# Kernel tuning notes

Measured on AMD Instinct MI355X. Metric: run time of the kernel, lower is better.

## Reference

```python
import jax, jax.numpy as jnp
import numpy as np

EPS = 1e-5  # torch LayerNorm default


def _ln(x, w, b):
    m = jnp.mean(x, axis=-1, keepdims=True)
    v = jnp.mean((x - m) ** 2, axis=-1, keepdims=True)
    return (x - m) / jnp.sqrt(v + EPS) * w + b


def _conv1x1(x, w, b):
    # x: [B,C,H,W], w: [O,C], b: [O]
    return jnp.einsum('bchw,oc->bohw', x, w) + b[None, :, None, None]


def setup_inputs() -> dict:
    key = jax.random.key(0)
    ks = jax.random.split(key, 5)
    B, Cin, H, W = 8, 384, 64, 64
    D, N = 128, 512
    s = lambda k, shape, scale=0.02: jax.random.normal(k, shape, jnp.float32) * scale
    return {
        'x': jax.random.normal(ks[0], (B, Cin, H, W), jnp.float32),
        'DR': jax.random.normal(ks[1], (N, D), jnp.float32),
        'conv_in_w': s(ks[2], (D, Cin)),
        'conv_in_b': jnp.zeros((D,), jnp.float32),
        'sem_w': s(ks[3], (D, D)),
        'sem_b': jnp.zeros((D,), jnp.float32),
        'norm1_w': jnp.ones((D,), jnp.float32),
        'norm1_b': jnp.zeros((D,), jnp.float32),
        'norm2_w': jnp.ones((D,), jnp.float32),
        'norm2_b': jnp.zeros((D,), jnp.float32),
        'conv_out_w': s(ks[4], (Cin, D)),
        'conv_out_b': jnp.zeros((Cin,), jnp.float32),
    }


def reference(x, DR, conv_in_w, conv_in_b, sem_w, sem_b, norm1_w, norm1_b,
              norm2_w, norm2_b, conv_out_w, conv_out_b):
    B, _, H, W = x.shape
    N = DR.shape[0]
    x_align = _conv1x1(x, conv_in_w, conv_in_b)                      # [B,D,H,W]
    x_sem = _conv1x1(x_align, sem_w, sem_b)                          # semantic_extra (1x1 conv)
    x_sem = x_sem.transpose(0, 2, 3, 1).reshape(B, H * W, -1)        # [B,HW,D]
    x_sem = _ln(x_sem, norm1_w, norm1_b)
    dr = _ln(DR, norm2_w, norm2_b).T                                 # [D,N] (same for all batches)
    # NOTE: original applies norm_1 TWICE for the numerator (faithful quirk)
    c_u = jnp.einsum('bld,dn->bln', _ln(x_sem, norm1_w, norm1_b), dr)  # [B,HW,N]
    c_d_l = jnp.sqrt(jnp.sum(x_sem ** 2, axis=-1, keepdims=True))      # [B,HW,1]
    c_d_r = jnp.sqrt(jnp.sum(dr ** 2, axis=0, keepdims=True))[None]    # [1,1,N]
    sim = c_u / (c_d_l * c_d_r)
    sim_soft = jax.nn.softmax(sim, axis=-1)                          # [B,HW,N]
    sim2d = sim_soft.transpose(0, 2, 1).reshape(B, N, H, W)
    degrad = jnp.einsum('bln,dn->bdl', sim_soft, dr).reshape(B, -1, H, W)  # [B,D,H,W]
    # pow-mask with per-batch min-max normalization
    mask_v = jnp.max(sim2d ** 3, axis=1, keepdims=True)              # [B,1,H,W]
    mn = jnp.min(mask_v.reshape(B, -1), axis=1).reshape(B, 1, 1, 1)
    mx = jnp.max(mask_v.reshape(B, -1), axis=1).reshape(B, 1, 1, 1)
    mask_v = 1.0 - (mask_v - mn) / (mx - mn)
    # topk row selection (torch fancy indexing gives [B,B,K,N]; squeeze(1) is a no-op for B>1)
    max_values = jnp.max(sim_soft, axis=2)                           # [B,HW]
    K = (H * W) // 50
    _, top_idx = jax.lax.top_k(max_values, K)                        # [B,K]
    results = jnp.take(sim_soft, top_idx, axis=1)                    # [B,B,K,N]
    out_img = _conv1x1(degrad, conv_out_w, conv_out_b)               # [B,Cin,H,W]
    return (mask_v, out_img, results)
```

## Files before the change

### kernel.cpp

```cpp
#include <hip/hip_runtime.h>
#include <cstdint>

#define EPS 1e-5f
#define BB   8
#define CIN  384
#define HWs  4096
#define LT   32768
#define DD   128
#define NN   512
#define TOPK 81

typedef short short8 __attribute__((ext_vector_type(8)));
typedef float f32x4  __attribute__((ext_vector_type(4)));

__device__ __forceinline__ unsigned short f2bf(float x) {
  unsigned u = __float_as_uint(x);
  u += 0x7fffu + ((u >> 16) & 1u);
  return (unsigned short)(u >> 16);
}
__device__ __forceinline__ float bf2f(unsigned u16) {
  return __uint_as_float(u16 << 16);
}
__device__ __forceinline__ void put_frag(unsigned short* buf, int tile, int rc, int k, float v) {
  int ks = k >> 5, g = (k >> 3) & 3, j = k & 7;
  int basehw = ((tile * 4 + ks) * 2) * 512 + (g * 16 + rc) * 8 + j;
  unsigned short hi = f2bf(v);
  buf[basehw] = hi;
  buf[basehw + 512] = f2bf(v - bf2f(hi));
}

__global__ __launch_bounds__(64) void k_dr(const float* __restrict__ DR,
    const float* __restrict__ w2, const float* __restrict__ b2,
    const float* __restrict__ w1, const float* __restrict__ b1,
    unsigned short* __restrict__ drwF, unsigned short* __restrict__ drlnF,
    float* __restrict__ t2, float* __restrict__ rcr) {
  int n = blockIdx.x;
  int lane = threadIdx.x;
  const float* row = DR + n * DD;
  float x0 = row[lane], x1 = row[lane + 64];
  float s = x0 + x1, sq = x0 * x0 + x1 * x1;
  #pragma unroll
  for (int o = 32; o; o >>= 1) { s += __shfl_xor(s, o); sq += __shfl_xor(sq, o); }
  float m = s * (1.f / 128.f);
  float v = sq * (1.f / 128.f) - m * m;
  float inv = rsqrtf(v + EPS);
  float y0 = (x0 - m) * inv * w2[lane] + b2[lane];
  float y1 = (x1 - m) * inv * w2[lane + 64] + b2[lane + 64];
  int nt = n >> 4, cc = n & 15;
  put_frag(drwF, nt, cc, lane, y0 * w1[lane]);
  put_frag(drwF, nt, cc, lane + 64, y1 * w1[lane + 64]);
  int ks = n >> 5, gB = (n >> 3) & 3, j = n & 7;
  {
    int d = lane;
    unsigned short hi = f2bf(y0);
    int base = (((d >> 4) * 16 + ks) * 2) * 512 + (gB * 16 + (d & 15)) * 8 + j;
    drlnF[base] = hi;
    drlnF[base + 512] = f2bf(y0 - bf2f(hi));
  }
  {
    int d = lane + 64;
    unsigned short hi = f2bf(y1);
    int base = (((d >> 4) * 16 + ks) * 2) * 512 + (gB * 16 + (d & 15)) * 8 + j;
    drlnF[base] = hi;
    drlnF[base + 512] = f2bf(y1 - bf2f(hi));
  }
  float pt2 = y0 * b1[lane] + y1 * b1[lane + 64];
  float pss = y0 * y0 + y1 * y1;
  #pragma unroll
  for (int o = 32; o; o >>= 1) { pt2 += __shfl_xor(pt2, o); pss += __shfl_xor(pss, o); }
  if (lane == 0) { t2[n] = pt2; rcr[n] = rsqrtf(pss); }
}

__global__ __launch_bounds__(256) void k_bprep(const float* __restrict__ src,
                                               unsigned short* __restrict__ dst,
                                               int K) {
  int rt = blockIdx.x, kb = blockIdx.y;
  int t = threadIdx.x, m = t >> 4, kg = t & 15;
  int k0 = kb * 128 + kg * 8;
  const float* s = src + (size_t)(rt * 16 + m) * K + k0;
  float4 f0 = *(const float4*)s;
  float4 f1 = *(const float4*)(s + 4);
  float vs[8] = {f0.x, f0.y, f0.z, f0.w, f1.x, f1.y, f1.z, f1.w};
  short8 hi, lo;
  #pragma unroll
  for (int j = 0; j < 8; ++j) {
    unsigned short h = f2bf(vs[j]);
    hi[j] = (short)h;
    lo[j] = (short)f2bf(vs[j] - bf2f(h));
  }
  int nkt = K >> 5;
  int ks = k0 >> 5, g = (k0 >> 3) & 3;
  short8* D8 = (short8*)dst;
  int base = ((rt * nkt + ks) * 2) * 64 + g * 16 + m;
  D8[base] = hi;
  D8[base + 64] = lo;
}

__global__ __launch_bounds__(256) void k_convin(const float* __restrict__ x,
    const unsigned short* __restrict__ WinF, const float* __restrict__ bias,
    unsigned short* __restrict__ xaF) {
  __shared__ float smem[64 * 132];
  int t = threadIdx.x;
  int w = t >> 6, lane = t & 63, m = lane & 15, g = lane >> 4;
  int l0 = blockIdx.x * 64;
  int b = l0 >> 12, hw0 = l0 & 4095;
  const float* xb = x + (size_t)b * CIN * HWs + hw0;
  const short8* B8 = (const short8*)WinF;
  f32x4 acc[4][2];
  #pragma unroll
  for (int lt = 0; lt < 4; ++lt)
    #pragma unroll
    for (int j2 = 0; j2 < 2; ++j2) acc[lt][j2] = (f32x4){0.f, 0.f, 0.f, 0.f};
  for (int ks = 0; ks < 12; ++ks) {
    short8 ah[4], al[4];
    const float* xc = xb + (size_t)(ks * 32 + g * 8) * HWs;
    #pragma unroll
    for (int lt = 0; lt < 4; ++lt) {
      const float* xcl = xc + lt * 16 + m;
      float v[8];
      #pragma unroll
      for (int j = 0; j < 8; ++j) v[j] = xcl[(size_t)j * HWs];
      #pragma unroll
      for (int j = 0; j < 8; ++j) {
        unsigned short h = f2bf(v[j]);
        ah[lt][j] = (short)h;
        al[lt][j] = (short)f2bf(v[j] - bf2f(h));
      }
    }
    #pragma unroll
    for (int j2 = 0; j2 < 2; ++j2) {
      int dt = w * 2 + j2;
      short8 bh = B8[((dt * 12 + ks) * 2 + 0) * 64 + lane];
      short8 bl = B8[((dt * 12 + ks) * 2 + 1) * 64 + lane];
      #pragma unroll
      for (int lt = 0; lt < 4; ++lt) {
        acc[lt][j2] = __builtin_amdgcn_mfma_f32_16x16x32_bf16(ah[lt], bh, acc[lt][j2], 0, 0, 0);
        acc[lt][j2] = __builtin_amdgcn_mfma_f32_16x16x32_bf16(ah[lt], bl, acc[lt][j2], 0, 0, 0);
        acc[lt][j2] = __builtin_amdgcn_mfma_f32_16x16x32_bf16(al[lt], bh, acc[lt][j2], 0, 0, 0);
      }
    }
  }
  float bia[2] = {bias[w * 32 + m], bias[w * 32 + 16 + m]};
  #pragma unroll
  for (int lt = 0; lt < 4; ++lt)
    #pragma unroll
    for (int j2 = 0; j2 < 2; ++j2)
      #pragma unroll
      for (int r = 0; r < 4; ++r)
        smem[(lt * 16 + g * 4 + r) * 132 + (w * 2 + j2) * 16 + m] = acc[lt][j2][r] + bia[j2];
  __syncthreads();
  short8* X8 = (short8*)xaF;
  #pragma unroll
  for (int it = 0; it < 4; ++it) {
    int idx = it * 256 + t;
    int l = idx & 63, dq = idx >> 6;
    const float* src = &smem[l * 132 + dq * 8];
    float4 f0 = *(const float4*)src;
    float4 f1 = *(const float4*)(src + 4);
    float vs[8] = {f0.x, f0.y, f0.z, f0.w, f1.x, f1.y, f1.z, f1.w};
    short8 hi, lo;
    #pragma unroll
    for (int j = 0; j < 8; ++j) {
      unsigned short h = f2bf(vs[j]);
      hi[j] = (short)h;
      lo[j] = (short)f2bf(vs[j] - bf2f(h));
    }
    int ltg = (l0 + l) >> 4;
    int idx8 = ((ltg * 4 + (dq >> 2)) * 2) * 64 + (dq & 3) * 16 + (l & 15);
    X8[idx8] = hi;
    X8[idx8 + 64] = lo;
  }
}

__global__ __launch_bounds__(256) void k_sem(const unsigned short* __restrict__ xaF,
    const unsigned short* __restrict__ semWF, const float* __restrict__ bias,
    const float* __restrict__ w1, const float* __restrict__ b1,
    unsigned short* __restrict__ ApF, float* __restrict__ rclv) {
  __shared__ float smem[64 * 132];
  __shared__ float sredS[64][4], sredQ[64][4];
  __shared__ float rowM[64], rowI[64];
  int t = threadIdx.x;
  int w = t >> 6, lane = t & 63, m = lane & 15, g = lane >> 4;
  int l0 = blockIdx.x * 64;
  int lt0 = l0 >> 4;
  const short8* A8 = (const short8*)xaF;
  const short8* B8 = (const short8*)semWF;
  f32x4 acc[4][2];
  #pragma unroll
  for (int lt = 0; lt < 4; ++lt)
    #pragma unroll
    for (int j2 = 0; j2 < 2; ++j2) acc[lt][j2] = (f32x4){0.f, 0.f, 0.f, 0.f};
  #pragma unroll
  for (int ks = 0; ks < 4; ++ks) {
    short8 ah[4], al[4];
    #pragma unroll
    for (int lt = 0; lt < 4; ++lt) {
      ah[lt] = A8[(((lt0 + lt) * 4 + ks) * 2 + 0) * 64 + lane];
      al[lt] = A8[(((lt0 + lt) * 4 + ks) * 2 + 1) * 64 + lane];
    }
    #pragma unroll
    for (int j2 = 0; j2 < 2; ++j2) {
      int dt = w * 2 + j2;
      short8 bh = B8[((dt * 4 + ks) * 2 + 0) * 64 + lane];
      short8 bl = B8[((dt * 4 + ks) * 2 + 1) * 64 + lane];
      #pragma unroll
      for (int lt = 0; lt < 4; ++lt) {
        acc[lt][j2] = __builtin_amdgcn_mfma_f32_16x16x32_bf16(ah[lt], bh, acc[lt][j2], 0, 0, 0);
        acc[lt][j2] = __builtin_amdgcn_mfma_f32_16x16x32_bf16(ah[lt], bl, acc[lt][j2], 0, 0, 0);
        acc[lt][j2] = __builtin_amdgcn_mfma_f32_16x16x32_bf16(al[lt], bh, acc[lt][j2], 0, 0, 0);
      }
    }
  }
  float bia[2] = {bias[w * 32 + m], bias[w * 32 + 16 + m]};
  #pragma unroll
  for (int lt = 0; lt < 4; ++lt)
    #pragma unroll
    for (int j2 = 0; j2 < 2; ++j2)
      #pragma unroll
      for (int r = 0; r < 4; ++r) acc[lt][j2][r] += bia[j2];
  float s1[4][4], q1[4][4];
  #pragma unroll
  for (int lt = 0; lt < 4; ++lt)
    #pragma unroll
    for (int r = 0; r < 4; ++r) {
      float a = acc[lt][0][r], b2v = acc[lt][1][r];
      s1[lt][r] = a + b2v;
      q1[lt][r] = a * a + b2v * b2v;
    }
  #pragma unroll
  for (int o = 1; o < 16; o <<= 1)
    #pragma unroll
    for (int lt = 0; lt < 4; ++lt)
      #pragma unroll
      for (int r = 0; r < 4; ++r) {
        s1[lt][r] += __shfl_xor(s1[lt][r], o);
        q1[lt][r] += __shfl_xor(q1[lt][r], o);
      }
  if (m == 0) {
    #pragma unroll
    for (int lt = 0; lt < 4; ++lt)
      #pragma unroll
      for (int r = 0; r < 4; ++r) {
        sredS[lt * 16 + g * 4 + r][w] = s1[lt][r];
        sredQ[lt * 16 + g * 4 + r][w] = q1[lt][r];
      }
  }
  __syncthreads();
  if (t < 64) {
    float S = sredS[t][0] + sredS[t][1] + sredS[t][2] + sredS[t][3];
    float Q = sredQ[t][0] + sredQ[t][1] + sredQ[t][2] + sredQ[t][3];
    float mu = S * (1.f / 128.f);
    float var = Q * (1.f / 128.f) - mu * mu;
    rowM[t] = mu;
    rowI[t] = rsqrtf(var + EPS);
  }
  __syncthreads();
  float w1v[2] = {w1[w * 32 + m], w1[w * 32 + 16 + m]};
  float b1v[2] = {b1[w * 32 + m], b1[w * 32 + 16 + m]};
  #pragma unroll
  for (int lt = 0; lt < 4; ++lt)
    #pragma unroll
    for (int r = 0; r < 4; ++r) {
      float mu = rowM[lt * 16 + g * 4 + r];
      float iv = rowI[lt * 16 + g * 4 + r];
      float y0 = (acc[lt][0][r] - mu) * iv * w1v[0] + b1v[0];
      float y1 = (acc[lt][1][r] - mu) * iv * w1v[1] + b1v[1];
      acc[lt][0][r] = y0; acc[lt][1][r] = y1;
      s1[lt][r] = y0 + y1;
      q1[lt][r] = y0 * y0 + y1 * y1;
    }
  #pragma unroll
  for (int o = 1; o < 16; o <<= 1)
    #pragma unroll
    for (int lt = 0; lt < 4; ++lt)
      #pragma unroll
      for (int r = 0; r < 4; ++r) {
        s1[lt][r] += __shfl_xor(s1[lt][r], o);
        q1[lt][r] += __shfl_xor(q1[lt][r], o);
      }
  if (m == 0) {
    #pragma unroll
    for (int lt = 0; lt < 4; ++lt)
      #pragma unroll
      for (int r = 0; r < 4; ++r) {
        sredS[lt * 16 + g * 4 + r][w] = s1[lt][r];
        sredQ[lt * 16 + g * 4 + r][w] = q1[lt][r];
      }
  }
  __syncthreads();
  if (t < 64) {
    float S = sredS[t][0] + sredS[t][1] + sredS[t][2] + sredS[t][3];
    float Q = sredQ[t][0] + sredQ[t][1] + sredQ[t][2] + sredQ[t][3];
    float m2 = S * (1.f / 128.f);
    float v2 = Q * (1.f / 128.f) - m2 * m2;
    float inv2 = rsqrtf(v2 + EPS);
    float rcl = rsqrtf(Q);
    rowM[t] = m2;
    rowI[t] = inv2 * rcl;
    rclv[l0 + t] = rcl;
  }
  __syncthreads();
  #pragma unroll
  for (int lt = 0; lt < 4; ++lt)
    #pragma unroll
    for (int r = 0; r < 4; ++r) {
      float m2 = rowM[lt * 16 + g * 4 + r];
      float sc = rowI[lt * 16 + g * 4 + r];
      smem[(lt * 16 + g * 4 + r) * 132 + w * 32 + m] = (acc[lt][0][r] - m2) * sc;
      smem[(lt * 16 + g * 4 + r) * 132 + w * 32 + 16 + m] = (acc[lt][1][r] - m2) * sc;
    }
  __syncthreads();
  short8* O8 = (short8*)ApF;
  #pragma unroll
  for (int it = 0; it < 4; ++it) {
    int idx = it * 256 + t;
    int l = idx & 63, dq = idx >> 6;
    const float* src = &smem[l * 132 + dq * 8];
    float4 f0 = *(const float4*)src;
    float4 f1 = *(const float4*)(src + 4);
    float vs[8] = {f0.x, f0.y, f0.z, f0.w, f1.x, f1.y, f1.z, f1.w};
    short8 hi, lo;
    #pragma unroll
    for (int j = 0; j < 8; ++j) {
      unsigned short h = f2bf(vs[j]);
      hi[j] = (short)h;
      lo[j] = (short)f2bf(vs[j] - bf2f(h));
    }
    int ltg = (l0 + l) >> 4;
    int idx8 = ((ltg * 4 + (dq >> 2)) * 2) * 64 + (dq & 3) * 16 + (l & 15);
    O8[idx8] = hi;
    O8[idx8 + 64] = lo;
  }
}

__global__ __launch_bounds__(256) void k_scores(const unsigned short* __restrict__ ApF,
    const unsigned short* __restrict__ drwF, const float* __restrict__ t2g,
    const float* __restrict__ rcrg, const float* __restrict__ rclg,
    unsigned short* __restrict__ pF, float* __restrict__ maxv) {
  __shared__ float sred[32][5];
  int t = threadIdx.x;
  int w = t >> 6, lane = t & 63, c = lane & 15, g = lane >> 4;
  int l0 = blockIdx.x * 32;
  int lt0 = blockIdx.x * 2;
  const short8* A8 = (const short8*)ApF;
  const short8* B8 = (const short8*)drwF;
  f32x4 acc[2][8];
  #pragma unroll
  for (int il = 0; il < 2; ++il)
    #pragma unroll
    for (int jn = 0; jn < 8; ++jn) acc[il][jn] = (f32x4){0.f, 0.f, 0.f, 0.f};
  #pragma unroll
  for (int ks = 0; ks < 4; ++ks) {
    short8 ah0 = A8[((lt0 * 4 + ks) * 2 + 0) * 64 + lane];
    short8 al0 = A8[((lt0 * 4 + ks) * 2 + 1) * 64 + lane];
    short8 ah1 = A8[(((lt0 + 1) * 4 + ks) * 2 + 0) * 64 + lane];
    short8 al1 = A8[(((lt0 + 1) * 4 + ks) * 2 + 1) * 64 + lane];
    #pragma unroll
    for (int jn = 0; jn < 8; ++jn) {
      int nt = w * 8 + jn;
      short8 bh = B8[((nt * 4 + ks) * 2 + 0) * 64 + lane];
      short8 bl = B8[((nt * 4 + ks) * 2 + 1) * 64 + lane];
      acc[0][jn] = __builtin_amdgcn_mfma_f32_16x16x32_bf16(ah0, bh, acc[0][jn], 0, 0, 0);
      acc[0][jn] = __builtin_amdgcn_mfma_f32_16x16x32_bf16(ah0, bl, acc[0][jn], 0, 0, 0);
      acc[0][jn] = __builtin_amdgcn_mfma_f32_16x16x32_bf16(al0, bh, acc[0][jn], 0, 0, 0);
      acc[1][jn] = __builtin_amdgcn_mfma_f32_16x16x32_bf16(ah1, bh, acc[1][jn], 0, 0, 0);
      acc[1][jn] = __builtin_amdgcn_mfma_f32_16x16x32_bf16(ah1, bl, acc[1][jn], 0, 0, 0);
      acc[1][jn] = __builtin_amdgcn_mfma_f32_16x16x32_bf16(al1, bh, acc[1][jn], 0, 0, 0);
    }
  }
  float rcrv[8], t2v[8];
  #pragma unroll
  for (int jn = 0; jn < 8; ++jn) {
    int n = w * 128 + jn * 16 + c;
    rcrv[jn] = rcrg[n]; t2v[jn] = t2g[n];
  }
  float rclr[2][4];
  #pragma unroll
  for (int il = 0; il < 2; ++il)
    #pragma unroll
    for (int r = 0; r < 4; ++r)
      rclr[il][r] = rclg[l0 + il * 16 + g * 4 + r];
  float M[2][4];
  #pragma unroll
  for (int il = 0; il < 2; ++il)
    #pragma unroll
    for (int r = 0; r < 4; ++r) M[il][r] = -1e30f;
  #pragma unroll
  for (int il = 0; il < 2; ++il)
    #pragma unroll
    for (int jn = 0; jn < 8; ++jn) {
      f32x4 a = acc[il][jn];
      #pragma unroll
      for (int r = 0; r < 4; ++r) {
        float s = rcrv[jn] * (a[r] + rclr[il][r] * t2v[jn]);
        a[r] = s;
        M[il][r] = fmaxf(M[il][r], s);
      }
      acc[il][jn] = a;
    }
  #pragma unroll
  for (int o = 1; o < 16; o <<= 1)
    #pragma unroll
    for (int il = 0; il < 2; ++il)
      #pragma unroll
      for (int r = 0; r < 4; ++r)
        M[il][r] = fmaxf(M[il][r], __shfl_xor(M[il][r], o));
  if (c == 0) {
    #pragma unroll
    for (int il = 0; il < 2; ++il)
      #pragma unroll
      for (int r = 0; r < 4; ++r)
        sred[il * 16 + g * 4 + r][w] = M[il][r];
  }
  __syncthreads();
  if (t < 32) {
    float mm = fmaxf(fmaxf(sred[t][0], sred[t][1]), fmaxf(sred[t][2], sred[t][3]));
    sred[t][4] = mm;
  }
  __syncthreads();
  float Mf[2][4];
  #pragma unroll
  for (int il = 0; il < 2; ++il)
    #pragma unroll
    for (int r = 0; r < 4; ++r)
      Mf[il][r] = sred[il * 16 + g * 4 + r][4];
  float S[2][4];
  #pragma unroll
  for (int il = 0; il < 2; ++il)
    #pragma unroll
    for (int r = 0; r < 4; ++r) S[il][r] = 0.f;
  #pragma unroll
  for (int il = 0; il < 2; ++il)
    #pragma unroll
    for (int jn = 0; jn < 8; ++jn) {
      f32x4 a = acc[il][jn];
      #pragma unroll
      for (int r = 0; r < 4; ++r) {
        float e = expf(a[r] - Mf[il][r]);
        a[r] = e;
        S[il][r] += e;
      }
      acc[il][jn] = a;
    }
  #pragma unroll
  for (int o = 1; o < 16; o <<= 1)
    #pragma unroll
    for (int il = 0; il < 2; ++il)
      #pragma unroll
      for (int r = 0; r < 4; ++r)
        S[il][r] += __shfl_xor(S[il][r], o);
  __syncthreads();
  if (c == 0) {
    #pragma unroll
    for (int il = 0; il < 2; ++il)
      #pragma unroll
      for (int r = 0; r < 4; ++r)
        sred[il * 16 + g * 4 + r][w] = S[il][r];
  }
  __syncthreads();
  if (t < 32) {
    float tot = sred[t][0] + sred[t][1] + sred[t][2] + sred[t][3];
    float rs = 1.f / tot;
    sred[t][4] = rs;
    maxv[l0 + t] = rs;
  }
  __syncthreads();
  #pragma unroll
  for (int il = 0; il < 2; ++il) {
    int lt = lt0 + il;
    #pragma unroll
    for (int r = 0; r < 4; ++r) {
      int mrow = g * 4 + r;
      float rs = sred[il * 16 + mrow][4];
      #pragma unroll
      for (int jn = 0; jn < 8; ++jn) {
        int ks = w * 4 + (jn >> 1);
        int gB = (jn * 2 + (c >> 3)) & 3;
        pF[((lt * 16 + ks) * 64 + gB * 16 + mrow) * 8 + (c & 7)] =
            f2bf(acc[il][jn][r] * rs);
      }
    }
  }
}

__global__ __launch_bounds__(256) void k_deg(const unsigned short* __restrict__ pF,
    const unsigned short* __restrict__ drlnF, const unsigned short* __restrict__ WoF,
    const float* __restrict__ bo, float* __restrict__ out_img) {
  __shared__ float smem[64 * 132];
  int t = threadIdx.x;
  int w = t >> 6, lane = t & 63, c = lane & 15, g = lane >> 4;
  int l0 = blockIdx.x * 64;
  int lt0 = l0 >> 4;
  const short8* P8 = (const short8*)pF;
  const short8* D8 = (const short8*)drlnF;
  const short8* W8 = (const short8*)WoF;
  f32x4 acc[4][2];
  #pragma unroll
  for (int lt = 0; lt < 4; ++lt)
    #pragma unroll
    for (int j2 = 0; j2 < 2; ++j2) acc[lt][j2] = (f32x4){0.f, 0.f, 0.f, 0.f};
  for (int ks = 0; ks < 16; ++ks) {
    short8 a0 = P8[((lt0 + 0) * 16 + ks) * 64 + lane];
    short8 a1 = P8[((lt0 + 1) * 16 + ks) * 64 + lane];
    short8 a2 = P8[((lt0 + 2) * 16 + ks) * 64 + lane];
    short8 a3 = P8[((lt0 + 3) * 16 + ks) * 64 + lane];
    #pragma unroll
    for (int j2 = 0; j2 < 2; ++j2) {
      int dt = w * 2 + j2;
      short8 bh = D8[((dt * 16 + ks) * 2 + 0) * 64 + lane];
      short8 bl = D8[((dt * 16 + ks) * 2 + 1) * 64 + lane];
      acc[0][j2] = __builtin_amdgcn_mfma_f32_16x16x32_bf16(a0, bh, acc[0][j2], 0, 0, 0);
      acc[0][j2] = __builtin_amdgcn_mfma_f32_16x16x32_bf16(a0, bl, acc[0][j2], 0, 0, 0);
      acc[1][j2] = __builtin_amdgcn_mfma_f32_16x16x32_bf16(a1, bh, acc[1][j2], 0, 0, 0);
      acc[1][j2] = __builtin_amdgcn_mfma_f32_16x16x32_bf16(a1, bl, acc[1][j2], 0, 0, 0);
      acc[2][j2] = __builtin_amdgcn_mfma_f32_16x16x32_bf16(a2, bh, acc[2][j2], 0, 0, 0);
      acc[2][j2] = __builtin_amdgcn_mfma_f32_16x16x32_bf16(a2, bl, acc[2][j2], 0, 0, 0);
      acc[3][j2] = __builtin_amdgcn_mfma_f32_16x16x32_bf16(a3, bh, acc[3][j2], 0, 0, 0);
      acc[3][j2] = __builtin_amdgcn_mfma_f32_16x16x32_bf16(a3, bl, acc[3][j2], 0, 0, 0);
    }
  }
  #pragma unroll
  for (int lt = 0; lt < 4; ++lt)
    #pragma unroll
    for (int j2 = 0; j2 < 2; ++j2)
      #pragma unroll
      for (int r = 0; r < 4; ++r)
        smem[(lt * 16 + g * 4 + r) * 132 + w * 32 + j2 * 16 + c] = acc[lt][j2][r];
  __syncthreads();
  f32x4 acc2[4][6];
  #pragma unroll
  for (int lt = 0; lt < 4; ++lt)
    #pragma unroll
    for (int ot = 0; ot < 6; ++ot) acc2[lt][ot] = (f32x4){0.f, 0.f, 0.f, 0.f};
  #pragma unroll
  for (int ks2 = 0; ks2 < 4; ++ks2) {
    short8 dh[4];
    #pragma unroll
    for (int lt = 0; lt < 4; ++lt) {
      const float* src = &smem[(lt * 16 + c) * 132 + ks2 * 32 + g * 8];
      float4 f0 = *(const float4*)src;
      float4 f1 = *(const float4*)(src + 4);
      float vs[8] = {f0.x, f0.y, f0.z, f0.w, f1.x, f1.y, f1.z, f1.w};
      #pragma unroll
      for (int j = 0; j < 8; ++j) dh[lt][j] = (short)f2bf(vs[j]);
    }
    #pragma unroll
    for (int ot = 0; ot < 6; ++ot) {
      int otg = w * 6 + ot;
      short8 wh = W8[((otg * 4 + ks2) * 2 + 0) * 64 + lane];
      short8 wl = W8[((otg * 4 + ks2) * 2 + 1) * 64 + lane];
      #pragma unroll
      for (int lt = 0; lt < 4; ++lt) {
        acc2[lt][ot] = __builtin_amdgcn_mfma_f32_16x16x32_bf16(dh[lt], wh, acc2[lt][ot], 0, 0, 0);
        acc2[lt][ot] = __builtin_amdgcn_mfma_f32_16x16x32_bf16(dh[lt], wl, acc2[lt][ot], 0, 0, 0);
      }
    }
  }
  __syncthreads();
  int b = l0 >> 12, hw0 = l0 & 4095;
  float* ob = out_img + (size_t)b * CIN * HWs + hw0;
  float bov[6];
  #pragma unroll
  for (int ot = 0; ot < 6; ++ot) bov[ot] = bo[w * 96 + ot * 16 + c];
  for (int ot = 0; ot < 6; ++ot) {
    #pragma unroll
    for (int lt = 0; lt < 4; ++lt)
      #pragma unroll
      for (int r = 0; r < 4; ++r)
        smem[(lt * 16 + g * 4 + r) * 65 + w * 16 + c] = acc2[lt][ot][r] + bov[ot];
    __syncthreads();
    #pragma unroll
    for (int i = 0; i < 16; ++i) {
      int idx = t + i * 256;
      int o_l = idx >> 6, ll = idx & 63;
      int o = (o_l >> 4) * 96 + ot * 16 + (o_l & 15);
      ob[(size_t)o * HWs + ll] = smem[ll * 65 + o_l];
    }
    __syncthreads();
  }
}

__global__ __launch_bounds__(256) void k_mask(const float* __restrict__ maxv,
                                              float* __restrict__ outm) {
  int b = blockIdx.x, t = threadIdx.x;
  float c[16];
  float mn = 1e30f, mx = -1e30f;
  #pragma unroll
  for (int j = 0; j < 16; ++j) {
    float x = maxv[b * HWs + t + j * 256];
    float cc = x * x * x;
    c[j] = cc;
    mn = fminf(mn, cc); mx = fmaxf(mx, cc);
  }
  #pragma unroll
  for (int o = 32; o; o >>= 1) { mn = fminf(mn, __shfl_xor(mn, o)); mx = fmaxf(mx, __shfl_xor(mx, o)); }
  __shared__ float smn[4], smx[4];
  int w = t >> 6;
  if ((t & 63) == 0) { smn[w] = mn; smx[w] = mx; }
  __syncthreads();
  mn = fminf(fminf(smn[0], smn[1]), fminf(smn[2], smn[3]));
  mx = fmaxf(fmaxf(smx[0], smx[1]), fmaxf(smx[2], smx[3]));
  float sc = 1.f / (mx - mn);
  #pragma unroll
  for (int j = 0; j < 16; ++j)
    outm[b * HWs + t + j * 256] = 1.f - (c[j] - mn) * sc;
}

__global__ __launch_bounds__(256) void k_topk(const float* __restrict__ maxv,
                                              int* __restrict__ tix) {
  __shared__ unsigned int hist[4][256];
  __shared__ unsigned long long slist[TOPK];
  __shared__ unsigned long long bc_prefix;
  __shared__ int bc_need, scount;
  int b = blockIdx.x, t = threadIdx.x;
  int w = t >> 6;
  unsigned long long key[16];
  #pragma unroll
  for (int j = 0; j < 16; ++j) {
    int idx = t + j * 256;
    unsigned int bits = __float_as_uint(maxv[b * HWs + idx]);
    key[j] = ((unsigned long long)bits << 12) | (unsigned)(4095 - idx);
  }
  if (t == 0) { bc_prefix = 0ull; bc_need = TOPK; scount = 0; }
  for (int r = 0; r < 6; ++r) {
    int shift = 40 - 8 * r;
    unsigned int* hflat = (unsigned int*)hist;
    hflat[t] = 0; hflat[t + 256] = 0; hflat[t + 512] = 0; hflat[t + 768] = 0;
    __syncthreads();
    unsigned long long prefix = bc_prefix;
    int bins[16];
    #pragma unroll
    for (int j = 0; j < 16; ++j)
      bins[j] = ((key[j] >> (shift + 8)) == prefix) ? (int)((key[j] >> shift) & 255) : -1;
    #pragma unroll
    for (int j = 0; j < 16; ++j) {
      if (bins[j] >= 0) {
        int cnt = 1;
        #pragma unroll
        for (int j2 = j + 1; j2 < 16; ++j2)
          if (bins[j2] == bins[j]) { bins[j2] = -1; ++cnt; }
        atomicAdd(&hist[w][bins[j]], (unsigned)cnt);
      }
    }
    __syncthreads();
    if (t < 64) {
      int cb[4], s = 0;
      #pragma unroll
      for (int j = 0; j < 4; ++j) {
        int bin = 255 - (t * 4 + j);
        cb[j] = (int)(hist[0][bin] + hist[1][bin] + hist[2][bin] + hist[3][bin]);
        s += cb[j];
      }
      int P = s;
      #pragma unroll
      for (int o = 1; o < 64; o <<= 1) {
        int u = __shfl_up(P, o);
        if (t >= o) P += u;
      }
      int need = bc_need;
      unsigned long long mask = __ballot(P >= need);
      int first = __ffsll((long long)mask) - 1;
      if (t == first) {
        int acc = P - s;
        #pragma unroll
        for (int j = 0; j < 4; ++j) {
          if (acc + cb[j] >= need) {
            bc_prefix = (prefix << 8) | (unsigned)(255 - (t * 4 + j));
            bc_need = need - acc;
            break;
          }
          acc += cb[j];
        }
      }
    }
    __syncthreads();
  }
  unsigned long long K81 = bc_prefix;
  #pragma unroll
  for (int j = 0; j < 16; ++j)
    if (key[j] >= K81) {
      int pos = atomicAdd(&scount, 1);
      slist[pos] = key[j];
    }
  __syncthreads();
  if (t < TOPK) {
    unsigned long long mine = slist[t];
    int rank = 0;
    for (int i = 0; i < TOPK; ++i) rank += (slist[i] > mine) ? 1 : 0;
    tix[b * TOPK + rank] = 4095 - (int)(mine & 0xFFFull);
  }
}

__global__ __launch_bounds__(128) void k_gather(const unsigned short* __restrict__ pF,
    const int* __restrict__ tix, float* __restrict__ outr) {
  int gB_ = blockIdx.x;
  int k = gB_ % TOPK;
  int bb = gB_ / TOPK;
  int b2 = bb & 7, b = bb >> 3;
  int l = b * HWs + tix[b2 * TOPK + k];
  int lt = l >> 4, mrow = l & 15;
  int t = threadIdx.x;
  int ks = t >> 3, gq = (t >> 1) & 3, j0 = (t & 1) * 4;
  int base = ((lt * 16 + ks) * 64 + gq * 16 + mrow) * 8 + j0;
  const unsigned* src = (const unsigned*)(pF + base);
  unsigned u0 = src[0], u1 = src[1];
  float4 v = {bf2f(u0 & 0xffffu), bf2f(u0 >> 16), bf2f(u1 & 0xffffu), bf2f(u1 >> 16)};
  *(float4*)(outr + (size_t)gB_ * NN + t * 4) = v;
}

extern "C" void kernel_launch(void* const* d_in, const int* in_sizes, int n_in,
                              void* d_out, int out_size, void* d_ws, size_t ws_size,
                              hipStream_t stream) {
  const float* x    = (const float*)d_in[0];
  const float* DR   = (const float*)d_in[1];
  const float* win  = (const float*)d_in[2];
  const float* bin  = (const float*)d_in[3];
  const float* sw   = (const float*)d_in[4];
  const float* sb   = (const float*)d_in[5];
  const float* n1w  = (const float*)d_in[6];
  const float* n1b  = (const float*)d_in[7];
  const float* n2w  = (const float*)d_in[8];
  const float* n2b  = (const float*)d_in[9];
  const float* wout = (const float*)d_in[10];
  const float* bout = (const float*)d_in[11];
  float* out = (float*)d_out;
  float* W = (float*)d_ws;

  unsigned short* drwF  = (unsigned short*)(W);
  float* t2   = W + 65536;
  float* rcr  = W + 66048;
  float* rclv = W + 66560;
  float* maxv = W + 99328;
  unsigned short* drlnF = (unsigned short*)(W + 132096);
  unsigned short* WoF   = (unsigned short*)(W + 197632);
  unsigned short* WinF  = (unsigned short*)(W + 246784);
  unsigned short* semWF = (unsigned short*)(W + 295936);
  unsigned short* ApF   = (unsigned short*)(W + 312320);
  unsigned short* xaF   = (unsigned short*)(W + 4506624);
  unsigned short* pF    = (unsigned short*)(W + 4506624);
  int*   tix  = (int*)(W + 12895232);

  float* out_mask = out;
  float* out_img  = out + 32768;
  float* out_res  = out + 32768 + 12582912;

  k_dr    <<<NN, 64, 0, stream>>>(DR, n2w, n2b, n1w, n1b, drwF, drlnF, t2, rcr);
  k_bprep <<<dim3(8, 3),  256, 0, stream>>>(win,  WinF,  CIN);
  k_bprep <<<dim3(8, 1),  256, 0, stream>>>(sw,   semWF, DD);
  k_bprep <<<dim3(24, 1), 256, 0, stream>>>(wout, WoF,   DD);
  k_convin<<<512,  256, 0, stream>>>(x, WinF, bin, xaF);
  k_sem   <<<512,  256, 0, stream>>>(xaF, semWF, sb, n1w, n1b, ApF, rclv);
  k_scores<<<1024, 256, 0, stream>>>(ApF, drwF, t2, rcr, rclv, pF, maxv);
  k_deg   <<<512,  256, 0, stream>>>(pF, drlnF, WoF, bout, out_img);
  k_mask  <<<BB,   256, 0, stream>>>(maxv, out_mask);
  k_topk  <<<BB,   256, 0, stream>>>(maxv, tix);
  k_gather<<<BB * BB * TOPK, 128, 0, stream>>>(pF, tix, out_res);
}
```

Baseline: 250.1 us.

## Fuse prep and mask/topk kernels, enlarge score tiles with LDS-staged output

Merges the DR layernorm kernel and the three weight-prep launches into one 184-block kernel, and merges the mask and top-k kernels into one, cutting launch count. The score kernel now handles 64 rows per block instead of 32, doubling reuse of the B fragments. It uses a single-pass online-softmax merge across waves in place of two separate barrier-separated reductions. Probabilities are staged in LDS and written out as coalesced 16-byte stores. The costs are higher register pressure from 32 accumulators, about 66KB of shared memory per block, and fewer blocks in the score grid.

Result: no change. 251.9 us (+0.7%).

```diff
diff --git a/kernel.cpp b/kernel.cpp
--- a/kernel.cpp
+++ b/kernel.cpp
@@ -29,53 +29,67 @@
   buf[basehw + 512] = f2bf(v - bf2f(hi));
 }
 
-__global__ __launch_bounds__(64) void k_dr(const float* __restrict__ DR,
+__global__ __launch_bounds__(256) void k_prep(const float* __restrict__ DR,
     const float* __restrict__ w2, const float* __restrict__ b2,
     const float* __restrict__ w1, const float* __restrict__ b1,
+    const float* __restrict__ win, const float* __restrict__ sw,
+    const float* __restrict__ wout,
     unsigned short* __restrict__ drwF, unsigned short* __restrict__ drlnF,
-    float* __restrict__ t2, float* __restrict__ rcr) {
-  int n = blockIdx.x;
-  int lane = threadIdx.x;
-  const float* row = DR + n * DD;
-  float x0 = row[lane], x1 = row[lane + 64];
-  float s = x0 + x1, sq = x0 * x0 + x1 * x1;
-  #pragma unroll
-  for (int o = 32; o; o >>= 1) { s += __shfl_xor(s, o); sq += __shfl_xor(sq, o); }
-  float m = s * (1.f / 128.f);
-  float v = sq * (1.f / 128.f) - m * m;
-  float inv = rsqrtf(v + EPS);
-  float y0 = (x0 - m) * inv * w2[lane] + b2[lane];
-  float y1 = (x1 - m) * inv * w2[lane + 64] + b2[lane + 64];
-  int nt = n >> 4, cc = n & 15;
-  put_frag(drwF, nt, cc, lane, y0 * w1[lane]);
-  put_frag(drwF, nt, cc, lane + 64, y1 * w1[lane + 64]);
-  int ks = n >> 5, gB = (n >> 3) & 3, j = n & 7;
-  {
-    int d = lane;
-    unsigned short hi = f2bf(y0);
-    int base = (((d >> 4) * 16 + ks) * 2) * 512 + (gB * 16 + (d & 15)) * 8 + j;
-    drlnF[base] = hi;
-    drlnF[base + 512] = f2bf(y0 - bf2f(hi));
-  }
-  {
-    int d = lane + 64;
-    unsigned short hi = f2bf(y1);
-    int base = (((d >> 4) * 16 + ks) * 2) * 512 + (gB * 16 + (d & 15)) * 8 + j;
-    drlnF[base] = hi;
-    drlnF[base + 512] = f2bf(y1 - bf2f(hi));
-  }
-  float pt2 = y0 * b1[lane] + y1 * b1[lane + 64];
-  float pss = y0 * y0 + y1 * y1;
-  #pragma unroll
-  for (int o = 32; o; o >>= 1) { pt2 += __shfl_xor(pt2, o); pss += __shfl_xor(pss, o); }
-  if (lane == 0) { t2[n] = pt2; rcr[n] = rsqrtf(pss); }
-}
-
-__global__ __launch_bounds__(256) void k_bprep(const float* __restrict__ src,
-                                               unsigned short* __restrict__ dst,
-                                               int K) {
-  int rt = blockIdx.x, kb = blockIdx.y;
-  int t = threadIdx.x, m = t >> 4, kg = t & 15;
+    float* __restrict__ t2, float* __restrict__ rcr,
+    unsigned short* __restrict__ WinF, unsigned short* __restrict__ semWF,
+    unsigned short* __restrict__ WoF) {
+  int blk = blockIdx.x;
+  int t = threadIdx.x;
+  if (blk < 128) {
+    int w = t >> 6, lane = t & 63;
+    int n = blk * 4 + w;
+    const float* row = DR + n * DD;
+    float x0 = row[lane], x1 = row[lane + 64];
+    float s = x0 + x1, sq = x0 * x0 + x1 * x1;
+    #pragma unroll
+    for (int o = 32; o; o >>= 1) { s += __shfl_xor(s, o); sq += __shfl_xor(sq, o); }
+    float m = s * (1.f / 128.f);
+    float v = sq * (1.f / 128.f) - m * m;
+    float inv = rsqrtf(v + EPS);
+    float y0 = (x0 - m) * inv * w2[lane] + b2[lane];
+    float y1 = (x1 - m) * inv * w2[lane + 64] + b2[lane + 64];
+    int nt = n >> 4, cc = n & 15;
+    put_frag(drwF, nt, cc, lane, y0 * w1[lane]);
+    put_frag(drwF, nt, cc, lane + 64, y1 * w1[lane + 64]);
+    int ks = n >> 5, gB = (n >> 3) & 3, j = n & 7;
+    {
+      int d = lane;
+      unsigned short hi = f2bf(y0);
+      int base = (((d >> 4) * 16 + ks) * 2) * 512 + (gB * 16 + (d & 15)) * 8 + j;
+      drlnF[base] = hi;
+      drlnF[base + 512] = f2bf(y0 - bf2f(hi));
+    }
+    {
+      int d = lane + 64;
+      unsigned short hi = f2bf(y1);
+      int base = (((d >> 4) * 16 + ks) * 2) * 512 + (gB * 16 + (d & 15)) * 8 + j;
+      drlnF[base] = hi;
+      drlnF[base + 512] = f2bf(y1 - bf2f(hi));
+    }
+    float pt2 = y0 * b1[lane] + y1 * b1[lane + 64];
+    float pss = y0 * y0 + y1 * y1;
+    #pragma unroll
+    for (int o = 32; o; o >>= 1) { pt2 += __shfl_xor(pt2, o); pss += __shfl_xor(pss, o); }
+    if (lane == 0) { t2[n] = pt2; rcr[n] = rsqrtf(pss); }
+    return;
+  }
+  const float* src;
+  unsigned short* dst;
+  int K, rt, kb = 0;
+  if (blk < 152) {
+    int idx = blk - 128;
+    rt = idx & 7; kb = idx >> 3; src = win; dst = WinF; K = CIN;
+  } else if (blk < 160) {
+    rt = blk - 152; src = sw; dst = semWF; K = DD;
+  } else {
+    rt = blk - 160; src = wout; dst = WoF; K = DD;
+  }
+  int m = t >> 4, kg = t & 15;
   int k0 = kb * 128 + kg * 8;
   const float* s = src + (size_t)(rt * 16 + m) * K + k0;
   float4 f0 = *(const float4*)s;
@@ -337,35 +351,38 @@
     const unsigned short* __restrict__ drwF, const float* __restrict__ t2g,
     const float* __restrict__ rcrg, const float* __restrict__ rclg,
     unsigned short* __restrict__ pF, float* __restrict__ maxv) {
-  __shared__ float sred[32][5];
+  __shared__ unsigned short pS[64 * 520];
+  __shared__ float sredM[64][4], sredS[64][4];
   int t = threadIdx.x;
   int w = t >> 6, lane = t & 63, c = lane & 15, g = lane >> 4;
-  int l0 = blockIdx.x * 32;
-  int lt0 = blockIdx.x * 2;
+  int l0 = blockIdx.x * 64;
+  int lt0 = blockIdx.x * 4;
   const short8* A8 = (const short8*)ApF;
   const short8* B8 = (const short8*)drwF;
-  f32x4 acc[2][8];
-  #pragma unroll
-  for (int il = 0; il < 2; ++il)
-    #pragma unroll
-    for (int jn = 0; jn < 8; ++jn) acc[il][jn] = (f32x4){0.f, 0.f, 0.f, 0.f};
+  f32x4 acc[4][8];
+  #pragma unroll
+  for (int lt = 0; lt < 4; ++lt)
+    #pragma unroll
+    for (int jn = 0; jn < 8; ++jn) acc[lt][jn] = (f32x4){0.f, 0.f, 0.f, 0.f};
   #pragma unroll
   for (int ks = 0; ks < 4; ++ks) {
-    short8 ah0 = A8[((lt0 * 4 + ks) * 2 + 0) * 64 + lane];
-    short8 al0 = A8[((lt0 * 4 + ks) * 2 + 1) * 64 + lane];
-    short8 ah1 = A8[(((lt0 + 1) * 4 + ks) * 2 + 0) * 64 + lane];
-    short8 al1 = A8[(((lt0 + 1) * 4 + ks) * 2 + 1) * 64 + lane];
+    short8 ah[4], al[4];
+    #pragma unroll
+    for (int lt = 0; lt < 4; ++lt) {
+      ah[lt] = A8[(((lt0 + lt) * 4 + ks) * 2 + 0) * 64 + lane];
+      al[lt] = A8[(((lt0 + lt) * 4 + ks) * 2 + 1) * 64 + lane];
+    }
     #pragma unroll
     for (int jn = 0; jn < 8; ++jn) {
       int nt = w * 8 + jn;
       short8 bh = B8[((nt * 4 + ks) * 2 + 0) * 64 + lane];
       short8 bl = B8[((nt * 4 + ks) * 2 + 1) * 64 + lane];
-      acc[0][jn] = __builtin_amdgcn_mfma_f32_16x16x32_bf16(ah0, bh, acc[0][jn], 0, 0, 0);
-      acc[0][jn] = __builtin_amdgcn_mfma_f32_16x16x32_bf16(ah0, bl, acc[0][jn], 0, 0, 0);
-      acc[0][jn] = __builtin_amdgcn_mfma_f32_16x16x32_bf16(al0, bh, acc[0][jn], 0, 0, 0);
-      acc[1][jn] = __builtin_amdgcn_mfma_f32_16x16x32_bf16(ah1, bh, acc[1][jn], 0, 0, 0);
-      acc[1][jn] = __builtin_amdgcn_mfma_f32_16x16x32_bf16(ah1, bl, acc[1][jn], 0, 0, 0);
-      acc[1][jn] = __builtin_amdgcn_mfma_f32_16x16x32_bf16(al1, bh, acc[1][jn], 0, 0, 0);
+      #pragma unroll
+      for (int lt = 0; lt < 4; ++lt) {
+        acc[lt][jn] = __builtin_amdgcn_mfma_f32_16x16x32_bf16(ah[lt], bh, acc[lt][jn], 0, 0, 0);
+        acc[lt][jn] = __builtin_amdgcn_mfma_f32_16x16x32_bf16(ah[lt], bl, acc[lt][jn], 0, 0, 0);
+        acc[lt][jn] = __builtin_amdgcn_mfma_f32_16x16x32_bf16(al[lt], bh, acc[lt][jn], 0, 0, 0);
+      }
     }
   }
   float rcrv[8], t2v[8];
@@ -374,112 +391,100 @@
     int n = w * 128 + jn * 16 + c;
     rcrv[jn] = rcrg[n]; t2v[jn] = t2g[n];
   }
-  float rclr[2][4];
-  #pragma unroll
-  for (int il = 0; il < 2; ++il)
+  float rclr[4][4];
+  #pragma unroll
+  for (int lt = 0; lt < 4; ++lt)
     #pragma unroll
     for (int r = 0; r < 4; ++r)
-      rclr[il][r] = rclg[l0 + il * 16 + g * 4 + r];
-  float M[2][4];
-  #pragma unroll
-  for (int il = 0; il < 2; ++il)
-    #pragma unroll
-    for (int r = 0; r < 4; ++r) M[il][r] = -1e30f;
-  #pragma unroll
-  for (int il = 0; il < 2; ++il)
+      rclr[lt][r] = rclg[l0 + lt * 16 + g * 4 + r];
+  float M[4][4], S[4][4];
+  #pragma unroll
+  for (int lt = 0; lt < 4; ++lt)
+    #pragma unroll
+    for (int r = 0; r < 4; ++r) M[lt][r] = -1e30f;
+  #pragma unroll
+  for (int lt = 0; lt < 4; ++lt)
     #pragma unroll
     for (int jn = 0; jn < 8; ++jn) {
-      f32x4 a = acc[il][jn];
+      f32x4 a = acc[lt][jn];
       #pragma unroll
       for (int r = 0; r < 4; ++r) {
-        float s = rcrv[jn] * (a[r] + rclr[il][r] * t2v[jn]);
+        float s = rcrv[jn] * (a[r] + rclr[lt][r] * t2v[jn]);
         a[r] = s;
-        M[il][r] = fmaxf(M[il][r], s);
-      }
-      acc[il][jn] = a;
+        M[lt][r] = fmaxf(M[lt][r], s);
+      }
+      acc[lt][jn] = a;
     }
   #pragma unroll
   for (int o = 1; o < 16; o <<= 1)
     #pragma unroll
-    for (int il = 0; il < 2; ++il)
+    for (int lt = 0; lt < 4; ++lt)
       #pragma unroll
       for (int r = 0; r < 4; ++r)
-        M[il][r] = fmaxf(M[il][r], __shfl_xor(M[il][r], o));
+        M[lt][r] = fmaxf(M[lt][r], __shfl_xor(M[lt][r], o));
+  #pragma unroll
+  for (int lt = 0; lt < 4; ++lt)
+    #pragma unroll
+    for (int r = 0; r < 4; ++r) S[lt][r] = 0.f;
+  #pragma unroll
+  for (int lt = 0; lt < 4; ++lt)
+    #pragma unroll
+    for (int jn = 0; jn < 8; ++jn) {
+      f32x4 a = acc[lt][jn];
+      #pragma unroll
+      for (int r = 0; r < 4; ++r) {
+        float e = expf(a[r] - M[lt][r]);
+        a[r] = e;
+        S[lt][r] += e;
+      }
+      acc[lt][jn] = a;
+    }
+  #pragma unroll
+  for (int o = 1; o < 16; o <<= 1)
+    #pragma unroll
+    for (int lt = 0; lt < 4; ++lt)
+      #pragma unroll
+      for (int r = 0; r < 4; ++r)
+        S[lt][r] += __shfl_xor(S[lt][r], o);
   if (c == 0) {
     #pragma unroll
-    for (int il = 0; il < 2; ++il)
-      #pragma unroll
-      for (int r = 0; r < 4; ++r)
-        sred[il * 16 + g * 4 + r][w] = M[il][r];
-  }
-  __syncthreads();
-  if (t < 32) {
-    float mm = fmaxf(fmaxf(sred[t][0], sred[t][1]), fmaxf(sred[t][2], sred[t][3]));
-    sred[t][4] = mm;
-  }
-  __syncthreads();
-  float Mf[2][4];
-  #pragma unroll
-  for (int il = 0; il < 2; ++il)
-    #pragma unroll
-    for (int r = 0; r < 4; ++r)
-      Mf[il][r] = sred[il * 16 + g * 4 + r][4];
-  float S[2][4];
-  #pragma unroll
-  for (int il = 0; il < 2; ++il)
-    #pragma unroll
-    for (int r = 0; r < 4; ++r) S[il][r] = 0.f;
-  #pragma unroll
-  for (int il = 0; il < 2; ++il)
-    #pragma unroll
-    for (int jn = 0; jn < 8; ++jn) {
-      f32x4 a = acc[il][jn];
+    for (int lt = 0; lt < 4; ++lt)
       #pragma unroll
       for (int r = 0; r < 4; ++r) {
-        float e = expf(a[r] - Mf[il][r]);
-        a[r] = e;
-        S[il][r] += e;
-      }
-      acc[il][jn] = a;
-    }
-  #pragma unroll
-  for (int o = 1; o < 16; o <<= 1)
-    #pragma unroll
-    for (int il = 0; il < 2; ++il)
-      #pragma unroll
-      for (int r = 0; r < 4; ++r)
-        S[il][r] += __shfl_xor(S[il][r], o);
-  __syncthreads();
-  if (c == 0) {
-    #pragma unroll
-    for (int il = 0; il < 2; ++il)
-      #pragma unroll
-      for (int r = 0; r < 4; ++r)
-        sred[il * 16 + g * 4 + r][w] = S[il][r];
-  }
-  __syncthreads();
-  if (t < 32) {
-    float tot = sred[t][0] + sred[t][1] + sred[t][2] + sred[t][3];
-    float rs = 1.f / tot;
-    sred[t][4] = rs;
-    maxv[l0 + t] = rs;
-  }
-  __syncthreads();
-  #pragma unroll
-  for (int il = 0; il < 2; ++il) {
-    int lt = lt0 + il;
+        sredM[lt * 16 + g * 4 + r][w] = M[lt][r];
+        sredS[lt * 16 + g * 4 + r][w] = S[lt][r];
+      }
+  }
+  __syncthreads();
+  #pragma unroll
+  for (int lt = 0; lt < 4; ++lt) {
     #pragma unroll
     for (int r = 0; r < 4; ++r) {
-      int mrow = g * 4 + r;
-      float rs = sred[il * 16 + mrow][4];
-      #pragma unroll
-      for (int jn = 0; jn < 8; ++jn) {
-        int ks = w * 4 + (jn >> 1);
-        int gB = (jn * 2 + (c >> 3)) & 3;
-        pF[((lt * 16 + ks) * 64 + gB * 16 + mrow) * 8 + (c & 7)] =
-            f2bf(acc[il][jn][r] * rs);
-      }
-    }
+      int row = lt * 16 + g * 4 + r;
+      float m0 = sredM[row][0], m1 = sredM[row][1], m2 = sredM[row][2], m3 = sredM[row][3];
+      float Mg = fmaxf(fmaxf(m0, m1), fmaxf(m2, m3));
+      float Sg = sredS[row][0] * expf(m0 - Mg) + sredS[row][1] * expf(m1 - Mg)
+               + sredS[row][2] * expf(m2 - Mg) + sredS[row][3] * expf(m3 - Mg);
+      float F = expf(M[lt][r] - Mg) / Sg;
+      #pragma unroll
+      for (int jn = 0; jn < 8; ++jn)
+        pS[row * 520 + w * 128 + jn * 16 + c] = f2bf(acc[lt][jn][r] * F);
+    }
+  }
+  if (t < 64) {
+    float m0 = sredM[t][0], m1 = sredM[t][1], m2 = sredM[t][2], m3 = sredM[t][3];
+    float Mg = fmaxf(fmaxf(m0, m1), fmaxf(m2, m3));
+    float Sg = sredS[t][0] * expf(m0 - Mg) + sredS[t][1] * expf(m1 - Mg)
+             + sredS[t][2] * expf(m2 - Mg) + sredS[t][3] * expf(m3 - Mg);
+    maxv[l0 + t] = 1.f / Sg;
+  }
+  __syncthreads();
+  short8* O8 = (short8*)pF + lt0 * 1024;
+  #pragma unroll
+  for (int i = 0; i < 16; ++i) {
+    int fl = t + i * 256;
+    int lt = fl >> 10, ks = (fl >> 6) & 15, gB = (fl >> 4) & 3, mrow = fl & 15;
+    O8[fl] = *(const short8*)&pS[(lt * 16 + mrow) * 520 + ks * 32 + gB * 8];
   }
 }
 
@@ -580,48 +585,41 @@
   }
 }
 
-__global__ __launch_bounds__(256) void k_mask(const float* __restrict__ maxv,
-                                              float* __restrict__ outm) {
-  int b = blockIdx.x, t = threadIdx.x;
-  float c[16];
-  float mn = 1e30f, mx = -1e30f;
-  #pragma unroll
-  for (int j = 0; j < 16; ++j) {
-    float x = maxv[b * HWs + t + j * 256];
-    float cc = x * x * x;
-    c[j] = cc;
-    mn = fminf(mn, cc); mx = fmaxf(mx, cc);
-  }
-  #pragma unroll
-  for (int o = 32; o; o >>= 1) { mn = fminf(mn, __shfl_xor(mn, o)); mx = fmaxf(mx, __shfl_xor(mx, o)); }
-  __shared__ float smn[4], smx[4];
-  int w = t >> 6;
-  if ((t & 63) == 0) { smn[w] = mn; smx[w] = mx; }
-  __syncthreads();
-  mn = fminf(fminf(smn[0], smn[1]), fminf(smn[2], smn[3]));
-  mx = fmaxf(fmaxf(smx[0], smx[1]), fmaxf(smx[2], smx[3]));
-  float sc = 1.f / (mx - mn);
-  #pragma unroll
-  for (int j = 0; j < 16; ++j)
-    outm[b * HWs + t + j * 256] = 1.f - (c[j] - mn) * sc;
-}
-
-__global__ __launch_bounds__(256) void k_topk(const float* __restrict__ maxv,
-                                              int* __restrict__ tix) {
+__global__ __launch_bounds__(256) void k_mtk(const float* __restrict__ maxv,
+                                             float* __restrict__ outm,
+                                             int* __restrict__ tix) {
   __shared__ unsigned int hist[4][256];
   __shared__ unsigned long long slist[TOPK];
   __shared__ unsigned long long bc_prefix;
   __shared__ int bc_need, scount;
+  __shared__ float smn[4], smx[4];
   int b = blockIdx.x, t = threadIdx.x;
   int w = t >> 6;
+  float val[16];
   unsigned long long key[16];
+  float mn = 1e30f, mx = -1e30f;
   #pragma unroll
   for (int j = 0; j < 16; ++j) {
     int idx = t + j * 256;
-    unsigned int bits = __float_as_uint(maxv[b * HWs + idx]);
-    key[j] = ((unsigned long long)bits << 12) | (unsigned)(4095 - idx);
-  }
+    float x = maxv[b * HWs + idx];
+    val[j] = x;
+    float cc = x * x * x;
+    mn = fminf(mn, cc); mx = fmaxf(mx, cc);
+    key[j] = ((unsigned long long)__float_as_uint(x) << 12) | (unsigned)(4095 - idx);
+  }
+  #pragma unroll
+  for (int o = 32; o; o >>= 1) { mn = fminf(mn, __shfl_xor(mn, o)); mx = fmaxf(mx, __shfl_xor(mx, o)); }
+  if ((t & 63) == 0) { smn[w] = mn; smx[w] = mx; }
   if (t == 0) { bc_prefix = 0ull; bc_need = TOPK; scount = 0; }
+  __syncthreads();
+  mn = fminf(fminf(smn[0], smn[1]), fminf(smn[2], smn[3]));
+  mx = fmaxf(fmaxf(smx[0], smx[1]), fmaxf(smx[2], smx[3]));
+  float sc = 1.f / (mx - mn);
+  #pragma unroll
+  for (int j = 0; j < 16; ++j) {
+    float cc = val[j] * val[j] * val[j];
+    outm[b * HWs + t + j * 256] = 1.f - (cc - mn) * sc;
+  }
   for (int r = 0; r < 6; ++r) {
     int shift = 40 - 8 * r;
     unsigned int* hflat = (unsigned int*)hist;
@@ -744,15 +742,12 @@
   float* out_img  = out + 32768;
   float* out_res  = out + 32768 + 12582912;
 
-  k_dr    <<<NN, 64, 0, stream>>>(DR, n2w, n2b, n1w, n1b, drwF, drlnF, t2, rcr);
-  k_bprep <<<dim3(8, 3),  256, 0, stream>>>(win,  WinF,  CIN);
-  k_bprep <<<dim3(8, 1),  256, 0, stream>>>(sw,   semWF, DD);
-  k_bprep <<<dim3(24, 1), 256, 0, stream>>>(wout, WoF,   DD);
+  k_prep  <<<184,  256, 0, stream>>>(DR, n2w, n2b, n1w, n1b, win, sw, wout,
+                                     drwF, drlnF, t2, rcr, WinF, semWF, WoF);
   k_convin<<<512,  256, 0, stream>>>(x, WinF, bin, xaF);
   k_sem   <<<512,  256, 0, stream>>>(xaF, semWF, sb, n1w, n1b, ApF, rclv);
-  k_scores<<<1024, 256, 0, stream>>>(ApF, drwF, t2, rcr, rclv, pF, maxv);
+  k_scores<<<512,  256, 0, stream>>>(ApF, drwF, t2, rcr, rclv, pF, maxv);
   k_deg   <<<512,  256, 0, stream>>>(pF, drlnF, WoF, bout, out_img);
-  k_mask  <<<BB,   256, 0, stream>>>(maxv, out_mask);
-  k_topk  <<<BB,   256, 0, stream>>>(maxv, tix);
+  k_mtk   <<<BB,   256, 0, stream>>>(maxv, out_mask, tix);
   k_gather<<<BB * BB * TOPK, 128, 0, stream>>>(pF, tix, out_res);
 }
```
